# Kernel tuning notes

Hardware: AMD Instinct MI355X
Metric: run time of the kernel (lower is better)

The kernel has to match this reference:

```python
import jax, jax.numpy as jnp
import numpy as np

B, L, H = 2, 2048, 1024
N_HEADS = 16
HEAD = H // N_HEADS
LN_EPS = 1e-12


def setup_inputs() -> dict:
    key = jax.random.key(0)
    ks = jax.random.split(key, 8)
    s = 1.0 / np.sqrt(H)
    return {
        "embeddings": jax.random.normal(ks[0], (B, L, H), dtype=jnp.float32),
        "mask": jnp.zeros((B, 1, 1, L), dtype=jnp.float32),
        "Wq": jax.random.normal(ks[1], (H, H), dtype=jnp.float32) * s,
        "bq": jnp.zeros((H,), dtype=jnp.float32),
        "Wk": jax.random.normal(ks[2], (H, H), dtype=jnp.float32) * s,
        "bk": jnp.zeros((H,), dtype=jnp.float32),
        "Wv": jax.random.normal(ks[3], (H, H), dtype=jnp.float32) * s,
        "bv": jnp.zeros((H,), dtype=jnp.float32),
        "Wo": jax.random.normal(ks[4], (H, H), dtype=jnp.float32) * s,
        "bo": jnp.zeros((H,), dtype=jnp.float32),
        "ln_gamma": jnp.ones((H,), dtype=jnp.float32),
        "ln_beta": jnp.zeros((H,), dtype=jnp.float32),
    }


def _layer_norm(x, gamma, beta):
    mu = jnp.mean(x, axis=-1, keepdims=True)
    var = jnp.mean(jnp.square(x - mu), axis=-1, keepdims=True)
    return (x - mu) * jax.lax.rsqrt(var + LN_EPS) * gamma + beta


def reference(embeddings, mask, Wq, bq, Wk, bk, Wv, bv, Wo, bo, ln_gamma, ln_beta):
    b, l, h = embeddings.shape
    # QKV projections, split heads -> [b, n_heads, l, head]
    def split_heads(x):
        return x.reshape(b, l, N_HEADS, HEAD).transpose(0, 2, 1, 3)
    q = split_heads(embeddings @ Wq + bq)
    k = split_heads(embeddings @ Wk + bk)
    v = split_heads(embeddings @ Wv + bv)
    # Faithful to source: energies use Q @ V^T, scaled by sqrt(n_heads)
    energies = jnp.einsum("bhqd,bhkd->bhqk", q, v) / np.sqrt(N_HEADS) + mask
    weights = jax.nn.softmax(energies, axis=3)
    # Faithful to source: attended = weights @ K
    attended = jnp.einsum("bhqk,bhkd->bhqd", weights, k)
    attended = attended.transpose(0, 2, 1, 3).reshape(b, l, h)
    # Residual feed-forward (BertSelfOutput style): dense + residual + LN
    out = attended @ Wo + bo
    return _layer_norm(out + embeddings, ln_gamma, ln_beta)
```

## Files before the change

### kernel.cpp

```cpp
#include <hip/hip_runtime.h>

#define LOG2E 1.44269504f
#define C_QSCALE 0.360673760f
#define C_SHIFT  34.6246810f
typedef unsigned short u16;
typedef short bf16x8 __attribute__((ext_vector_type(8)));
typedef float f32x4 __attribute__((ext_vector_type(4)));
typedef unsigned short u16x4 __attribute__((ext_vector_type(4)));

#define BB 2
#define LL 2048
#define HH 1024
#define NH 16
#define HD 64
#define ML (BB*LL)

__device__ __forceinline__ u16 f2bf(float f) {
  union { float f; unsigned u; } v; v.f = f;
  unsigned r = v.u + 0x7FFFu + ((v.u >> 16) & 1u);
  return (u16)(r >> 16);
}
__device__ __forceinline__ u16 f2bf_trunc(float f) {
  union { float f; unsigned u; } v; v.f = f;
  return (u16)(v.u >> 16);
}
__device__ __forceinline__ float bf2f(u16 u) {
  union { unsigned u; float f; } v; v.u = ((unsigned)u) << 16;
  return v.f;
}
__device__ __forceinline__ void gload_lds16(const u16* g, u16* l) {
  __builtin_amdgcn_global_load_lds((const __attribute__((address_space(1))) void*)g,
                                   (__attribute__((address_space(3))) void*)l, 16, 0, 0);
}

__global__ __launch_bounds__(256) void k_prep(const float* __restrict__ E, u16* __restrict__ X,
                                              const float* W0, const float* W1,
                                              const float* W2, const float* W3,
                                              u16* __restrict__ WT) {
  __shared__ __align__(16) u16 T[64*72];
  if (blockIdx.x < 2048) {
    int idx = (blockIdx.x * 256 + threadIdx.x) * 8;
    float4 a = *(const float4*)(E + idx);
    float4 b = *(const float4*)(E + idx + 4);
    bf16x8 o;
    o[0]=f2bf(a.x); o[1]=f2bf(a.y); o[2]=f2bf(a.z); o[3]=f2bf(a.w);
    o[4]=f2bf(b.x); o[5]=f2bf(b.y); o[6]=f2bf(b.z); o[7]=f2bf(b.w);
    *(bf16x8*)(X + idx) = o;
    return;
  }
  int bz = blockIdx.x - 2048;
  int z = bz >> 8, rem = bz & 255, bx = rem & 15, by = rem >> 4;
  const float* W = (z==0)?W0:(z==1)?W1:(z==2)?W2:W3;
  u16* dst = WT + (size_t)z * HH * HH;
  int t = threadIdx.x;
  int n0 = bx * 64, k0 = by * 64;
  int kl = t >> 2, nc = t & 3;
  #pragma unroll
  for (int u = 0; u < 4; ++u) {
    float4 v = *(const float4*)(W + (size_t)(k0 + kl) * HH + n0 + nc*16 + u*4);
    int nb = nc*16 + u*4;
    T[(nb+0)*72 + kl] = f2bf(v.x);
    T[(nb+1)*72 + kl] = f2bf(v.y);
    T[(nb+2)*72 + kl] = f2bf(v.z);
    T[(nb+3)*72 + kl] = f2bf(v.w);
  }
  __syncthreads();
  int nl = t >> 2, kc = (t & 3) * 16;
  #pragma unroll
  for (int e = 0; e < 2; ++e) {
    bf16x8 v = *(const bf16x8*)(T + nl*72 + kc + e*8);
    *(bf16x8*)(dst + (size_t)(n0+nl)*HH + k0 + kc + e*8) = v;
  }
}

__global__ __launch_bounds__(256) void k_gemm(const u16* __restrict__ A, const u16* __restrict__ Bt,
                                              const float* __restrict__ b0, const float* __restrict__ b1,
                                              const float* __restrict__ b2,
                                              u16* __restrict__ QH, u16* __restrict__ KV) {
  __shared__ __align__(16) u16 As[2][128*32];
  __shared__ __align__(16) u16 Bs[2][128*32];
  int tid = threadIdx.x;
  int lane = tid & 63, w = tid >> 6;
  int c = lane & 15, g = lane >> 4;
  int bn0 = blockIdx.x * 128, bm0 = blockIdx.y * 128;
  int wm0 = (w >> 1) * 64, wn0 = (w & 1) * 64;
  int z = bn0 >> 10;
  bool swapd = (z != 1);
  const u16* srcA = swapd ? Bt : A;
  const u16* srcB = swapd ? A : Bt;
  int baseA = swapd ? bn0 : bm0;
  int baseB = swapd ? bm0 : bn0;

  f32x4 acc[4][4];
  #pragma unroll
  for (int mt = 0; mt < 4; ++mt)
    #pragma unroll
    for (int nt = 0; nt < 4; ++nt)
      acc[mt][nt] = (f32x4){0.f,0.f,0.f,0.f};

  #pragma unroll
  for (int it = 0; it < 2; ++it) {
    int ch = tid + it*256, row = ch >> 2, col = (ch & 3) * 8;
    gload_lds16(srcA + (size_t)(baseA + row) * HH + col, &As[0][ch*8]);
    gload_lds16(srcB + (size_t)(baseB + row) * HH + col, &Bs[0][ch*8]);
  }
  for (int kt = 0; kt < 32; ++kt) {
    __syncthreads();
    int cb = kt & 1;
    if (kt < 31) {
      int k0 = (kt + 1) * 32, nb = (kt + 1) & 1;
      #pragma unroll
      for (int it = 0; it < 2; ++it) {
        int ch = tid + it*256, row = ch >> 2, col = (ch & 3) * 8;
        gload_lds16(srcA + (size_t)(baseA + row) * HH + k0 + col, &As[nb][ch*8]);
        gload_lds16(srcB + (size_t)(baseB + row) * HH + k0 + col, &Bs[nb][ch*8]);
      }
    }
    bf16x8 af[4], bfr[4];
    #pragma unroll
    for (int i = 0; i < 4; ++i) {
      af[i]  = *(const bf16x8*)(&As[cb][0] + (wm0 + i*16 + c)*32 + g*8);
      bfr[i] = *(const bf16x8*)(&Bs[cb][0] + (wn0 + i*16 + c)*32 + g*8);
    }
    #pragma unroll
    for (int mt = 0; mt < 4; ++mt)
      #pragma unroll
      for (int nt = 0; nt < 4; ++nt)
        acc[mt][nt] = __builtin_amdgcn_mfma_f32_16x16x32_bf16(af[mt], bfr[nt], acc[mt][nt], 0, 0, 0);
  }

  if (z == 1) {
    #pragma unroll
    for (int nt = 0; nt < 4; ++nt) {
      int n = bn0 + wn0 + nt*16 + c;
      int nn = n & 1023, h = nn >> 6, d = nn & 63;
      float bv = b1[nn];
      #pragma unroll
      for (int mt = 0; mt < 4; ++mt) {
        int m0 = bm0 + wm0 + mt*16 + 4*g;
        int b = m0 >> 11, keyl = m0 & 2047;
        int tt = keyl >> 6, chunk = (keyl >> 3) & 7, s = keyl & 7;
        u16x4 pk;
        #pragma unroll
        for (int r = 0; r < 4; ++r) pk[r] = f2bf(acc[mt][nt][r] + bv);
        *(u16x4*)(KV + ((size_t)((b*NH + h)*32 + tt))*8192 + d*64 + ((chunk ^ (d & 7))*8) + s) = pk;
      }
    }
  } else {
    #pragma unroll
    for (int mt = 0; mt < 4; ++mt) {
      int nidx0 = bn0 + wm0 + mt*16 + 4*g;
      int nn0 = nidx0 & 1023, h = nn0 >> 6, d0 = nn0 & 63;
      const float* bp = (z == 0) ? b0 : b2;
      float4 bv = *(const float4*)(bp + nn0);
      #pragma unroll
      for (int nt = 0; nt < 4; ++nt) {
        int tok = bm0 + wn0 + nt*16 + c;
        int b = tok >> 11, l = tok & 2047;
        u16x4 o;
        o[0] = f2bf(acc[mt][nt][0] + bv.x);
        o[1] = f2bf(acc[mt][nt][1] + bv.y);
        o[2] = f2bf(acc[mt][nt][2] + bv.z);
        o[3] = f2bf(acc[mt][nt][3] + bv.w);
        if (z == 0) {
          *(u16x4*)(QH + (((size_t)(b*NH + h)) * LL + l) * HD + d0) = o;
        } else {
          int tt = l >> 6;
          *(u16x4*)(KV + ((size_t)((b*NH + h)*32 + tt))*8192 + 4096
                    + (l & 63)*64 + (((d0 >> 3) ^ (l & 7))*8) + (d0 & 7)) = o;
        }
      }
    }
  }
}

__global__ __launch_bounds__(256) void k_gemm_o(const u16* __restrict__ ATT, const u16* __restrict__ Wt,
                                                const float* __restrict__ bias,
                                                float* __restrict__ outf) {
  __shared__ __align__(16) u16 As[2][128*32];
  __shared__ __align__(16) u16 Bs[2][64*32];
  int tid = threadIdx.x;
  int lane = tid & 63, w = tid >> 6;
  int c = lane & 15, g = lane >> 4;
  int bn0 = blockIdx.x * 128, bm0 = blockIdx.y * 64;
  int wm0 = (w >> 1) * 64, wn0 = (w & 1) * 32;

  f32x4 acc[4][2];
  #pragma unroll
  for (int mt = 0; mt < 4; ++mt)
    #pragma unroll
    for (int nt = 0; nt < 2; ++nt)
      acc[mt][nt] = (f32x4){0.f,0.f,0.f,0.f};

  #pragma unroll
  for (int it = 0; it < 2; ++it) {
    int ch = tid + it*256, row = ch >> 2, col = (ch & 3) * 8;
    gload_lds16(Wt + (size_t)(bn0 + row) * HH + col, &As[0][ch*8]);
  }
  { int row = tid >> 2, col = (tid & 3) * 8;
    gload_lds16(ATT + (size_t)(bm0 + row) * HH + col, &Bs[0][tid*8]); }

  for (int kt = 0; kt < 32; ++kt) {
    __syncthreads();
    int cb = kt & 1;
    if (kt < 31) {
      int k0 = (kt + 1) * 32, nb = (kt + 1) & 1;
      #pragma unroll
      for (int it = 0; it < 2; ++it) {
        int ch = tid + it*256, row = ch >> 2, col = (ch & 3) * 8;
        gload_lds16(Wt + (size_t)(bn0 + row) * HH + k0 + col, &As[nb][ch*8]);
      }
      int row = tid >> 2, col = (tid & 3) * 8;
      gload_lds16(ATT + (size_t)(bm0 + row) * HH + k0 + col, &Bs[nb][tid*8]);
    }
    bf16x8 af[4], bfr[2];
    #pragma unroll
    for (int i = 0; i < 4; ++i)
      af[i] = *(const bf16x8*)(&As[cb][0] + (wm0 + i*16 + c)*32 + g*8);
    #pragma unroll
    for (int j = 0; j < 2; ++j)
      bfr[j] = *(const bf16x8*)(&Bs[cb][0] + (wn0 + j*16 + c)*32 + g*8);
    #pragma unroll
    for (int mt = 0; mt < 4; ++mt)
      #pragma unroll
      for (int nt = 0; nt < 2; ++nt)
        acc[mt][nt] = __builtin_amdgcn_mfma_f32_16x16x32_bf16(af[mt], bfr[nt], acc[mt][nt], 0, 0, 0);
  }
  #pragma unroll
  for (int mt = 0; mt < 4; ++mt) {
    int n0 = bn0 + wm0 + mt*16 + 4*g;
    float4 bv = *(const float4*)(bias + n0);
    #pragma unroll
    for (int nt = 0; nt < 2; ++nt) {
      int tok = bm0 + wn0 + nt*16 + c;
      float4 o;
      o.x = acc[mt][nt][0] + bv.x;
      o.y = acc[mt][nt][1] + bv.y;
      o.z = acc[mt][nt][2] + bv.z;
      o.w = acc[mt][nt][3] + bv.w;
      *(float4*)(outf + (size_t)tok * HH + n0) = o;
    }
  }
}

__global__ __launch_bounds__(256) void k_attn(const u16* __restrict__ QH, const u16* __restrict__ KV,
                                              const float* __restrict__ mask,
                                              u16* __restrict__ PO0, u16* __restrict__ PO1,
                                              float* __restrict__ PL) {
  __shared__ __align__(16) u16 sKV[8192];
  __shared__ __align__(16) u16 sP[4][32*72];
  int tid = threadIdx.x;
  int lane = tid & 63, w = tid >> 6;
  int c = lane & 15, g = lane >> 4;
  int z = blockIdx.y;
  int bh = blockIdx.z, b = bh >> 4;
  int q0 = blockIdx.x * 128 + w * 32;
  size_t qbase = (size_t)bh * LL * HD;
  const u16* kvg = KV + (size_t)bh * 32 * 8192 + (size_t)z * 16 * 8192;
  const float* mptr = mask + b * LL + z * 1024;
  u16* pw = &sP[w][0];

  bf16x8 aq[2][2];
  #pragma unroll
  for (int qi = 0; qi < 2; ++qi)
    #pragma unroll
    for (int ks = 0; ks < 2; ++ks)
      aq[qi][ks] = *(const bf16x8*)(QH + qbase + (size_t)(q0 + qi*16 + c) * HD + ks*32 + g*8);

  bf16x8 ones;
  #pragma unroll
  for (int i = 0; i < 8; ++i) ones[i] = (short)0x3F80;

  f32x4 O[2][4], lac[2];
  #pragma unroll
  for (int qi = 0; qi < 2; ++qi) {
    lac[qi] = (f32x4){0.f,0.f,0.f,0.f};
    #pragma unroll
    for (int dt = 0; dt < 4; ++dt) O[qi][dt] = (f32x4){0.f,0.f,0.f,0.f};
  }

  for (int tt = 0; tt < 16; ++tt) {
    __syncthreads();
    #pragma unroll
    for (int it = 0; it < 4; ++it) {
      int i = (tid + it*256) * 8;
      gload_lds16(kvg + (size_t)tt*8192 + i, sKV + i);
    }
    __syncthreads();

    int kv0 = tt * 64;
    #pragma unroll
    for (int nt = 0; nt < 4; ++nt) {
      int vrow = nt*16 + c;
      bf16x8 vb0 = *(const bf16x8*)(sKV + 4096 + vrow*64 + ((g ^ (c & 7))*8));
      bf16x8 vb1 = *(const bf16x8*)(sKV + 4096 + vrow*64 + (((4 + g) ^ (c & 7))*8));
      float mterm = fmaf(mptr[kv0 + vrow], LOG2E, -C_SHIFT);
      #pragma unroll
      for (int qi = 0; qi < 2; ++qi) {
        f32x4 sa = (f32x4){0.f,0.f,0.f,0.f};
        sa = __builtin_amdgcn_mfma_f32_16x16x32_bf16(aq[qi][0], vb0, sa, 0,0,0);
        sa = __builtin_amdgcn_mfma_f32_16x16x32_bf16(aq[qi][1], vb1, sa, 0,0,0);
        #pragma unroll
        for (int r = 0; r < 4; ++r)
          pw[(qi*16 + 4*g + r)*72 + nt*16 + c] = f2bf_trunc(exp2f(fmaf(sa[r], C_QSCALE, mterm)));
      }
    }
    bf16x8 ap[2][2];
    #pragma unroll
    for (int qi = 0; qi < 2; ++qi) {
      ap[qi][0] = *(const bf16x8*)(pw + (qi*16 + c)*72 + g*8);
      ap[qi][1] = *(const bf16x8*)(pw + (qi*16 + c)*72 + 32 + g*8);
      lac[qi] = __builtin_amdgcn_mfma_f32_16x16x32_bf16(ones, ap[qi][0], lac[qi], 0,0,0);
      lac[qi] = __builtin_amdgcn_mfma_f32_16x16x32_bf16(ones, ap[qi][1], lac[qi], 0,0,0);
    }
    #pragma unroll
    for (int dt = 0; dt < 4; ++dt) {
      int d = dt*16 + c;
      bf16x8 bk0 = *(const bf16x8*)(sKV + d*64 + ((g ^ (c & 7))*8));
      bf16x8 bk1 = *(const bf16x8*)(sKV + d*64 + (((4 + g) ^ (c & 7))*8));
      #pragma unroll
      for (int qi = 0; qi < 2; ++qi) {
        O[qi][dt] = __builtin_amdgcn_mfma_f32_16x16x32_bf16(bk0, ap[qi][0], O[qi][dt], 0,0,0);
        O[qi][dt] = __builtin_amdgcn_mfma_f32_16x16x32_bf16(bk1, ap[qi][1], O[qi][dt], 0,0,0);
      }
    }
  }
  u16* POp = (z == 0) ? PO0 : PO1;
  #pragma unroll
  for (int qi = 0; qi < 2; ++qi) {
    int q = q0 + qi*16 + c;
    size_t qrow = (size_t)bh * LL + q;
    if (g == 0) PL[(size_t)(z*32 + bh) * LL + q] = lac[qi][0];
    #pragma unroll
    for (int dt = 0; dt < 4; ++dt) {
      u16x4 o;
      #pragma unroll
      for (int r = 0; r < 4; ++r) o[r] = f2bf(O[qi][dt][r]);
      *(u16x4*)(POp + qrow*HD + dt*16 + 4*g) = o;
    }
  }
}

__global__ __launch_bounds__(256) void k_combine(const u16* __restrict__ PO0,
                                                 const u16* __restrict__ PO1,
                                                 const float* __restrict__ PL,
                                                 u16* __restrict__ ATT) {
  int bh = blockIdx.y, b = bh >> 4, h = bh & 15;
  int q = blockIdx.x * 128 + (threadIdx.x >> 1);
  int dh = (threadIdx.x & 1) * 32;
  size_t r0 = ((size_t)bh * LL + q) * HD + dh;
  float inv = 1.0f / (PL[(size_t)bh * LL + q] + PL[(size_t)(32 + bh) * LL + q]);
  u16* dst = ATT + ((size_t)(b*LL + q)) * HH + h*HD + dh;
  #pragma unroll
  for (int e = 0; e < 4; ++e) {
    bf16x8 a0 = *(const bf16x8*)(PO0 + r0 + e*8);
    bf16x8 a1 = *(const bf16x8*)(PO1 + r0 + e*8);
    bf16x8 o;
    #pragma unroll
    for (int i = 0; i < 8; ++i)
      o[i] = (short)f2bf((bf2f((u16)a0[i]) + bf2f((u16)a1[i])) * inv);
    *(bf16x8*)(dst + e*8) = o;
  }
}

__global__ __launch_bounds__(256) void k_ln(const float* __restrict__ OF, const float* __restrict__ E,
                                            const float* __restrict__ gamma, const float* __restrict__ beta,
                                            float* __restrict__ out) {
  int row = blockIdx.x;
  int tid = threadIdx.x, lane = tid & 63, w = tid >> 6;
  size_t basei = (size_t)row * HH + tid*4;
  float4 a = *(const float4*)(OF + basei);
  float4 e = *(const float4*)(E + basei);
  float x0 = a.x + e.x, x1 = a.y + e.y, x2 = a.z + e.z, x3 = a.w + e.w;
  float s1 = x0+x1+x2+x3;
  float s2 = x0*x0+x1*x1+x2*x2+x3*x3;
  #pragma unroll
  for (int off = 32; off; off >>= 1) { s1 += __shfl_xor(s1, off); s2 += __shfl_xor(s2, off); }
  __shared__ float r1[4], r2[4];
  if (lane == 0) { r1[w] = s1; r2[w] = s2; }
  __syncthreads();
  s1 = r1[0]+r1[1]+r1[2]+r1[3];
  s2 = r2[0]+r2[1]+r2[2]+r2[3];
  float mu = s1 * (1.0f/HH);
  float var = s2 * (1.0f/HH) - mu*mu;
  float rs = rsqrtf(fmaxf(var, 0.f) + 1e-12f);
  int colb = tid*4;
  float4 gm = *(const float4*)(gamma + colb);
  float4 bt = *(const float4*)(beta + colb);
  float4 o;
  o.x = (x0-mu)*rs*gm.x + bt.x;
  o.y = (x1-mu)*rs*gm.y + bt.y;
  o.z = (x2-mu)*rs*gm.z + bt.z;
  o.w = (x3-mu)*rs*gm.w + bt.w;
  *(float4*)(out + basei) = o;
}

extern "C" void kernel_launch(void* const* d_in, const int* in_sizes, int n_in,
                              void* d_out, int out_size, void* d_ws, size_t ws_size,
                              hipStream_t stream) {
  const float* E    = (const float*)d_in[0];
  const float* mask = (const float*)d_in[1];
  const float* Wq   = (const float*)d_in[2];
  const float* bq   = (const float*)d_in[3];
  const float* Wk   = (const float*)d_in[4];
  const float* bk   = (const float*)d_in[5];
  const float* Wv   = (const float*)d_in[6];
  const float* bv   = (const float*)d_in[7];
  const float* Wo   = (const float*)d_in[8];
  const float* bo   = (const float*)d_in[9];
  const float* gam  = (const float*)d_in[10];
  const float* bet  = (const float*)d_in[11];

  const size_t MH = (size_t)ML * HH;
  u16* XBF = (u16*)d_ws;
  u16* WT  = XBF + MH;
  u16* QH  = WT + 4*(size_t)HH*HH;
  u16* KV  = QH + MH;
  u16* ATT = KV + 2*MH;
  u16* PO0 = ATT + MH;
  u16* PO1 = PO0 + MH;
  float* out = (float*)d_out;
  float* PL = out;
  float* OF = (float*)PO0;

  k_prep<<<dim3(3072), 256, 0, stream>>>(E, XBF, Wq, Wk, Wv, Wo, WT);
  k_gemm<<<dim3(24,32), 256, 0, stream>>>(XBF, WT, bq, bk, bv, QH, KV);
  k_attn<<<dim3(16,2,32), 256, 0, stream>>>(QH, KV, mask, PO0, PO1, PL);
  k_combine<<<dim3(16,32), 256, 0, stream>>>(PO0, PO1, PL, ATT);
  k_gemm_o<<<dim3(8,64), 256, 0, stream>>>(ATT, WT + 3*(size_t)HH*HH, bo, OF);
  k_ln<<<dim3(ML), 256, 0, stream>>>(OF, E, gam, bet, out);
}
```

Measured before the change: 239.5 us.

## Double-buffer K/V tiles and keep softmax probabilities in registers via permlane swaps

The attention kernel now double-buffers the K/V tile in LDS: the next tile's global-to-LDS loads are issued before the current tile is computed, and one barrier per iteration is removed. The probability tile is no longer written to and read back from per-wave LDS. It is packed with v_cvt_pk_bf16_f32 and rearranged into the MFMA operand layout with permlane16/32 swaps, which required swapping the QK^T MFMA operand order. It also remaps block indices to change which blocks run together (likely for cache locality across dies), loads the mask as a float4, and raises the launch-bounds occupancy hint. The risks are that overlap depends on load completion being handled correctly at the barrier, and that probability rounding changes from truncation to round-to-nearest.

```diff
diff --git a/kernel.cpp b/kernel.cpp
--- a/kernel.cpp
+++ b/kernel.cpp
@@ -7,6 +7,7 @@
 typedef short bf16x8 __attribute__((ext_vector_type(8)));
 typedef float f32x4 __attribute__((ext_vector_type(4)));
 typedef unsigned short u16x4 __attribute__((ext_vector_type(4)));
+typedef unsigned int u32x4 __attribute__((ext_vector_type(4)));
 
 #define BB 2
 #define LL 2048
@@ -31,6 +32,17 @@
 __device__ __forceinline__ void gload_lds16(const u16* g, u16* l) {
   __builtin_amdgcn_global_load_lds((const __attribute__((address_space(1))) void*)g,
                                    (__attribute__((address_space(3))) void*)l, 16, 0, 0);
+}
+__device__ __forceinline__ unsigned cvt_pk_bf16(float lo, float hi) {
+  unsigned r;
+  asm("v_cvt_pk_bf16_f32 %0, %1, %2" : "=v"(r) : "v"(lo), "v"(hi));
+  return r;
+}
+__device__ __forceinline__ void pl16swap(unsigned &a, unsigned &b) {
+  asm("v_permlane16_swap_b32 %0, %1" : "+v"(a), "+v"(b));
+}
+__device__ __forceinline__ void pl32swap(unsigned &a, unsigned &b) {
+  asm("v_permlane32_swap_b32 %0, %1" : "+v"(a), "+v"(b));
 }
 
 __global__ __launch_bounds__(256) void k_prep(const float* __restrict__ E, u16* __restrict__ X,
@@ -243,22 +255,23 @@
   }
 }
 
-__global__ __launch_bounds__(256) void k_attn(const u16* __restrict__ QH, const u16* __restrict__ KV,
+__global__ __launch_bounds__(256, 4) void k_attn(const u16* __restrict__ QH, const u16* __restrict__ KV,
                                               const float* __restrict__ mask,
                                               u16* __restrict__ PO0, u16* __restrict__ PO1,
                                               float* __restrict__ PL) {
-  __shared__ __align__(16) u16 sKV[8192];
-  __shared__ __align__(16) u16 sP[4][32*72];
+  __shared__ __align__(16) u16 sKV[2][8192];
   int tid = threadIdx.x;
   int lane = tid & 63, w = tid >> 6;
   int c = lane & 15, g = lane >> 4;
-  int z = blockIdx.y;
-  int bh = blockIdx.z, b = bh >> 4;
-  int q0 = blockIdx.x * 128 + w * 32;
+  int phys = blockIdx.x + (blockIdx.y << 4) + (blockIdx.z << 5);
+  int virt = (phys & 7) * 128 + (phys >> 3);
+  int bx = virt & 15;
+  int z = (virt >> 4) & 1;
+  int bh = virt >> 5, b = bh >> 4;
+  int q0 = bx * 128 + w * 32;
   size_t qbase = (size_t)bh * LL * HD;
   const u16* kvg = KV + (size_t)bh * 32 * 8192 + (size_t)z * 16 * 8192;
   const float* mptr = mask + b * LL + z * 1024;
-  u16* pw = &sP[w][0];
 
   bf16x8 aq[2][2];
   #pragma unroll
@@ -279,45 +292,69 @@
     for (int dt = 0; dt < 4; ++dt) O[qi][dt] = (f32x4){0.f,0.f,0.f,0.f};
   }
 
+  #pragma unroll
+  for (int it = 0; it < 4; ++it) {
+    int i = (tid + it*256) * 8;
+    gload_lds16(kvg + i, &sKV[0][0] + i);
+  }
+
   for (int tt = 0; tt < 16; ++tt) {
     __syncthreads();
-    #pragma unroll
-    for (int it = 0; it < 4; ++it) {
-      int i = (tid + it*256) * 8;
-      gload_lds16(kvg + (size_t)tt*8192 + i, sKV + i);
-    }
-    __syncthreads();
-
+    int cb = tt & 1;
+    if (tt < 15) {
+      #pragma unroll
+      for (int it = 0; it < 4; ++it) {
+        int i = (tid + it*256) * 8;
+        gload_lds16(kvg + (size_t)(tt+1)*8192 + i, &sKV[cb^1][0] + i);
+      }
+    }
+    const u16* kvp = &sKV[cb][0];
     int kv0 = tt * 64;
+
+    unsigned X[2][4][2];
     #pragma unroll
     for (int nt = 0; nt < 4; ++nt) {
       int vrow = nt*16 + c;
-      bf16x8 vb0 = *(const bf16x8*)(sKV + 4096 + vrow*64 + ((g ^ (c & 7))*8));
-      bf16x8 vb1 = *(const bf16x8*)(sKV + 4096 + vrow*64 + (((4 + g) ^ (c & 7))*8));
-      float mterm = fmaf(mptr[kv0 + vrow], LOG2E, -C_SHIFT);
+      bf16x8 vb0 = *(const bf16x8*)(kvp + 4096 + vrow*64 + ((g ^ (c & 7))*8));
+      bf16x8 vb1 = *(const bf16x8*)(kvp + 4096 + vrow*64 + (((4 + g) ^ (c & 7))*8));
+      float4 mv = *(const float4*)(mptr + kv0 + nt*16 + 4*g);
+      float mt0 = fmaf(mv.x, LOG2E, -C_SHIFT);
+      float mt1 = fmaf(mv.y, LOG2E, -C_SHIFT);
+      float mt2 = fmaf(mv.z, LOG2E, -C_SHIFT);
+      float mt3 = fmaf(mv.w, LOG2E, -C_SHIFT);
       #pragma unroll
       for (int qi = 0; qi < 2; ++qi) {
         f32x4 sa = (f32x4){0.f,0.f,0.f,0.f};
-        sa = __builtin_amdgcn_mfma_f32_16x16x32_bf16(aq[qi][0], vb0, sa, 0,0,0);
-        sa = __builtin_amdgcn_mfma_f32_16x16x32_bf16(aq[qi][1], vb1, sa, 0,0,0);
-        #pragma unroll
-        for (int r = 0; r < 4; ++r)
-          pw[(qi*16 + 4*g + r)*72 + nt*16 + c] = f2bf_trunc(exp2f(fmaf(sa[r], C_QSCALE, mterm)));
+        sa = __builtin_amdgcn_mfma_f32_16x16x32_bf16(vb0, aq[qi][0], sa, 0,0,0);
+        sa = __builtin_amdgcn_mfma_f32_16x16x32_bf16(vb1, aq[qi][1], sa, 0,0,0);
+        float p0 = exp2f(fmaf(sa[0], C_QSCALE, mt0));
+        float p1 = exp2f(fmaf(sa[1], C_QSCALE, mt1));
+        float p2 = exp2f(fmaf(sa[2], C_QSCALE, mt2));
+        float p3 = exp2f(fmaf(sa[3], C_QSCALE, mt3));
+        X[qi][nt][0] = cvt_pk_bf16(p0, p1);
+        X[qi][nt][1] = cvt_pk_bf16(p2, p3);
       }
     }
     bf16x8 ap[2][2];
     #pragma unroll
     for (int qi = 0; qi < 2; ++qi) {
-      ap[qi][0] = *(const bf16x8*)(pw + (qi*16 + c)*72 + g*8);
-      ap[qi][1] = *(const bf16x8*)(pw + (qi*16 + c)*72 + 32 + g*8);
-      lac[qi] = __builtin_amdgcn_mfma_f32_16x16x32_bf16(ones, ap[qi][0], lac[qi], 0,0,0);
-      lac[qi] = __builtin_amdgcn_mfma_f32_16x16x32_bf16(ones, ap[qi][1], lac[qi], 0,0,0);
+      #pragma unroll
+      for (int h = 0; h < 2; ++h) {
+        unsigned x0 = X[qi][2*h][0],   x1 = X[qi][2*h][1];
+        unsigned x2 = X[qi][2*h+1][0], x3 = X[qi][2*h+1][1];
+        pl32swap(x0, x2); pl16swap(x0, x2);
+        pl32swap(x1, x3); pl16swap(x1, x3);
+        union { u32x4 u; bf16x8 b; } cvt;
+        cvt.u[0] = x0; cvt.u[1] = x1; cvt.u[2] = x2; cvt.u[3] = x3;
+        ap[qi][h] = cvt.b;
+        lac[qi] = __builtin_amdgcn_mfma_f32_16x16x32_bf16(ones, ap[qi][h], lac[qi], 0,0,0);
+      }
     }
     #pragma unroll
     for (int dt = 0; dt < 4; ++dt) {
       int d = dt*16 + c;
-      bf16x8 bk0 = *(const bf16x8*)(sKV + d*64 + ((g ^ (c & 7))*8));
-      bf16x8 bk1 = *(const bf16x8*)(sKV + d*64 + (((4 + g) ^ (c & 7))*8));
+      bf16x8 bk0 = *(const bf16x8*)(kvp + d*64 + ((g ^ (c & 7))*8));
+      bf16x8 bk1 = *(const bf16x8*)(kvp + d*64 + (((4 + g) ^ (c & 7))*8));
       #pragma unroll
       for (int qi = 0; qi < 2; ++qi) {
         O[qi][dt] = __builtin_amdgcn_mfma_f32_16x16x32_bf16(bk0, ap[qi][0], O[qi][dt], 0,0,0);
```

After: 235.8 us. About the same (-1.5%).
